# Kernel optimization log

Measured on AMD Instinct MI355X. Metric: run time of the kernel, lower is better.

Reference implementation:

```python
import jax, jax.numpy as jnp
import numpy as np


def setup_inputs() -> dict:
    key = jax.random.key(0)
    x = jax.random.normal(key, (64, 64, 16384), dtype=jnp.float32)
    return {"input_": x, "topk": 128}


def reference(input_, topk):
    # top-k by absolute value along the last axis; zero everything else
    B_shape = input_.shape[:-1]
    L = input_.shape[-1]
    _, idx = jax.lax.top_k(jnp.abs(input_), topk)          # [..., k] indices
    vals = jnp.take_along_axis(input_, idx, axis=-1)        # original signed values
    # flatten leading dims for a single batched scatter
    xf_rows = int(np.prod(B_shape))
    idx2 = idx.reshape(xf_rows, topk)
    vals2 = vals.reshape(xf_rows, topk)
    out = jnp.zeros((xf_rows, L), dtype=input_.dtype)
    rows = jnp.arange(xf_rows)[:, None]
    out = out.at[rows, idx2].set(vals2)
    return out.reshape(*B_shape, L)
```

## Files before the change

kernel.cpp:

```cpp
#include <hip/hip_runtime.h>
#include <stdint.h>

#define ROWLEN 16384
#define NT 512
#define VPT 8

typedef uint32_t uint32x4 __attribute__((ext_vector_type(4)));

#define SYNC_LDS() do { \
    asm volatile("s_waitcnt lgkmcnt(0)" ::: "memory"); \
    __builtin_amdgcn_s_barrier(); \
} while (0)

template <int NB>
__device__ __forceinline__ void select_bin(const uint32_t* __restrict__ hist,
                                           uint32_t* __restrict__ s_part,
                                           uint32_t* s_bin, int* s_kk, int* s_ceq,
                                           int kk, int tid)
{
    constexpr int C = NB / NT;
    uint32_t s = 0;
    #pragma unroll
    for (int j = 0; j < C; ++j) s += hist[tid * C + j];
    s_part[tid] = s;
    SYNC_LDS();
    if (tid < 64) {
        uint32_t g = 0;
        #pragma unroll
        for (int j = 0; j < 8; ++j) g += s_part[tid * 8 + j];
        uint32_t S = g;
        #pragma unroll
        for (int off = 1; off < 64; off <<= 1) {
            uint32_t o = __shfl_down(S, off, 64);
            if (tid + off < 64) S += o;
        }
        unsigned long long m = __ballot(S >= (uint32_t)kk);
        int c = 63 - __builtin_clzll(m);
        uint32_t hv = __shfl(S, (c + 1) & 63, 64);
        uint32_t higher = (c == 63) ? 0u : hv;
        if (tid == 0) {
            uint32_t pp[8];
            #pragma unroll
            for (int j = 0; j < 8; ++j) pp[j] = s_part[c * 8 + j];
            int kk2 = kk - (int)higher;
            int cum = 0, j = 7;
            #pragma unroll
            for (int it = 7; it > 0; --it) {
                int cc = (int)pp[j];
                if (cum + cc >= kk2) break;
                cum += cc; --j;
            }
            int tt = c * 8 + j;
            int kk3 = kk2 - cum;
            uint32_t bb[C];
            #pragma unroll
            for (int jj = 0; jj < C; ++jj) bb[jj] = hist[tt * C + jj];
            int cum2 = 0, b = C - 1;
            #pragma unroll
            for (int it = C - 1; it > 0; --it) {
                int cc = (int)bb[b];
                if (cum2 + cc >= kk3) break;
                cum2 += cc; --b;
            }
            *s_bin = (uint32_t)(tt * C + b);
            *s_kk  = kk3 - cum2;
            *s_ceq = (int)bb[b];
        }
    }
    SYNC_LDS();
}

__global__ __launch_bounds__(NT, 6) void topk_abs_kernel(
    const uint32_t* __restrict__ x, const int* __restrict__ kptr,
    uint32_t* __restrict__ out)
{
    __shared__ uint32_t hist[2048];
    __shared__ uint32_t s_part[NT];
    __shared__ uint32_t s_bin;
    __shared__ int s_kk, s_ceq, s_cnt;

    const int tid = threadIdx.x;
    const uint4* __restrict__ xr  = (const uint4*)(x   + (size_t)blockIdx.x * ROWLEN);
    uint32x4* __restrict__ outr   = (uint32x4*)   (out + (size_t)blockIdx.x * ROWLEN);
    const int k = *kptr;

    uint4 v[VPT];
    #pragma unroll
    for (int i = 0; i < VPT; ++i) v[i] = xr[i * NT + tid];

    hist[tid] = 0; hist[tid + 512] = 0; hist[tid + 1024] = 0; hist[tid + 1536] = 0;
    SYNC_LDS();
    #pragma unroll
    for (int i = 0; i < VPT; ++i) {
        atomicAdd(&hist[(v[i].x & 0x7FFFFFFFu) >> 20], 1u);
        atomicAdd(&hist[(v[i].y & 0x7FFFFFFFu) >> 20], 1u);
        atomicAdd(&hist[(v[i].z & 0x7FFFFFFFu) >> 20], 1u);
        atomicAdd(&hist[(v[i].w & 0x7FFFFFFFu) >> 20], 1u);
    }
    SYNC_LDS();
    select_bin<2048>(hist, s_part, &s_bin, &s_kk, &s_ceq, k, tid);
    const uint32_t b0 = s_bin;
    int kk = s_kk;
    const int ceq0 = s_ceq;

    hist[tid] = 0; hist[tid + 512] = 0;
    if (tid == 0) s_cnt = 0;
    SYNC_LDS();

    uint32_t T; int e, ceqT;
    if (ceq0 <= 1024) {
        uint32_t* cand = hist + 1024;
        #pragma unroll
        for (int i = 0; i < VPT; ++i) {
            uint32_t a;
            a = v[i].x & 0x7FFFFFFFu; if ((a >> 20) == b0) { cand[atomicAdd(&s_cnt, 1)] = a; atomicAdd(&hist[(a >> 10) & 1023u], 1u); }
            a = v[i].y & 0x7FFFFFFFu; if ((a >> 20) == b0) { cand[atomicAdd(&s_cnt, 1)] = a; atomicAdd(&hist[(a >> 10) & 1023u], 1u); }
            a = v[i].z & 0x7FFFFFFFu; if ((a >> 20) == b0) { cand[atomicAdd(&s_cnt, 1)] = a; atomicAdd(&hist[(a >> 10) & 1023u], 1u); }
            a = v[i].w & 0x7FFFFFFFu; if ((a >> 20) == b0) { cand[atomicAdd(&s_cnt, 1)] = a; atomicAdd(&hist[(a >> 10) & 1023u], 1u); }
        }
        SYNC_LDS();
        select_bin<1024>(hist, s_part, &s_bin, &s_kk, &s_ceq, kk, tid);
        const uint32_t b1 = s_bin;
        kk = s_kk;
        hist[tid] = 0; hist[tid + 512] = 0;
        SYNC_LDS();
        for (int t = tid; t < ceq0; t += NT) {
            uint32_t a = cand[t];
            if (((a >> 10) & 1023u) == b1) atomicAdd(&hist[a & 1023u], 1u);
        }
        SYNC_LDS();
        select_bin<1024>(hist, s_part, &s_bin, &s_kk, &s_ceq, kk, tid);
        T = (b0 << 20) | (b1 << 10) | s_bin;
        e = s_kk; ceqT = s_ceq;
    } else {
        #pragma unroll
        for (int i = 0; i < VPT; ++i) {
            uint32_t a;
            a = v[i].x & 0x7FFFFFFFu; if ((a >> 20) == b0) atomicAdd(&hist[(a >> 10) & 1023u], 1u);
            a = v[i].y & 0x7FFFFFFFu; if ((a >> 20) == b0) atomicAdd(&hist[(a >> 10) & 1023u], 1u);
            a = v[i].z & 0x7FFFFFFFu; if ((a >> 20) == b0) atomicAdd(&hist[(a >> 10) & 1023u], 1u);
            a = v[i].w & 0x7FFFFFFFu; if ((a >> 20) == b0) atomicAdd(&hist[(a >> 10) & 1023u], 1u);
        }
        SYNC_LDS();
        select_bin<1024>(hist, s_part, &s_bin, &s_kk, &s_ceq, kk, tid);
        const uint32_t b1 = s_bin;
        kk = s_kk;
        hist[tid] = 0; hist[tid + 512] = 0;
        SYNC_LDS();
        const uint32_t pfx = (b0 << 10) | b1;
        #pragma unroll
        for (int i = 0; i < VPT; ++i) {
            uint32_t a;
            a = v[i].x & 0x7FFFFFFFu; if ((a >> 10) == pfx) atomicAdd(&hist[a & 1023u], 1u);
            a = v[i].y & 0x7FFFFFFFu; if ((a >> 10) == pfx) atomicAdd(&hist[a & 1023u], 1u);
            a = v[i].z & 0x7FFFFFFFu; if ((a >> 10) == pfx) atomicAdd(&hist[a & 1023u], 1u);
            a = v[i].w & 0x7FFFFFFFu; if ((a >> 10) == pfx) atomicAdd(&hist[a & 1023u], 1u);
        }
        SYNC_LDS();
        select_bin<1024>(hist, s_part, &s_bin, &s_kk, &s_ceq, kk, tid);
        T = (b0 << 20) | (b1 << 10) | s_bin;
        e = s_kk; ceqT = s_ceq;
    }

    const bool rare = (ceqT != e);
    int nc = 0;
    if (rare) {
        if (tid == 0) s_cnt = 0;
        SYNC_LDS();
        #pragma unroll
        for (int i = 0; i < VPT; ++i) {
            uint32_t p4 = (uint32_t)(4 * (i * NT + tid));
            if ((v[i].x & 0x7FFFFFFFu) == T) { int q = atomicAdd(&s_cnt, 1); if (q < 1024) hist[q] = p4 + 0u; }
            if ((v[i].y & 0x7FFFFFFFu) == T) { int q = atomicAdd(&s_cnt, 1); if (q < 1024) hist[q] = p4 + 1u; }
            if ((v[i].z & 0x7FFFFFFFu) == T) { int q = atomicAdd(&s_cnt, 1); if (q < 1024) hist[q] = p4 + 2u; }
            if ((v[i].w & 0x7FFFFFFFu) == T) { int q = atomicAdd(&s_cnt, 1); if (q < 1024) hist[q] = p4 + 3u; }
        }
        SYNC_LDS();
        nc = s_cnt; if (nc > 1024) nc = 1024;
        for (int t = tid; t < nc; t += NT) {
            uint32_t my = hist[t];
            int rank = 0;
            for (int j = 0; j < nc; ++j) rank += (hist[j] < my) ? 1 : 0;
            hist[1024 + t] = (rank < e) ? 1u : 0u;
        }
        SYNC_LDS();
    }

    auto filt = [&](uint32_t bits, uint32_t idx) -> uint32_t {
        uint32_t key = bits & 0x7FFFFFFFu;
        if (key > T) return bits;
        if (key < T) return 0u;
        if (!rare) return bits;
        for (int j = 0; j < nc; ++j)
            if (hist[j] == idx) return hist[1024 + j] ? bits : 0u;
        return 0u;
    };
    #pragma unroll
    for (int i = 0; i < VPT; ++i) {
        int p = i * NT + tid;
        uint32_t p4 = (uint32_t)(4 * p);
        uint32x4 o;
        o.x = filt(v[i].x, p4 + 0u);
        o.y = filt(v[i].y, p4 + 1u);
        o.z = filt(v[i].z, p4 + 2u);
        o.w = filt(v[i].w, p4 + 3u);
        __builtin_nontemporal_store(o, &outr[p]);
    }
}

extern "C" void kernel_launch(void* const* d_in, const int* in_sizes, int n_in,
                              void* d_out, int out_size, void* d_ws, size_t ws_size,
                              hipStream_t stream) {
    const uint32_t* x = (const uint32_t*)d_in[0];
    const int* kptr   = (const int*)d_in[1];
    uint32_t* out     = (uint32_t*)d_out;
    const int rows = in_sizes[0] / ROWLEN;
    topk_abs_kernel<<<rows, NT, 0, stream>>>(x, kptr, out);
}
```

Before: 95.62 us.

## Use persistent blocks that prefetch the next row while processing the current

Switches from one block per row to a grid of at most 768 persistent blocks that loop over rows. Each block loads the next row into a second register buffer before running the histogram/select pipeline on the current row, so global load latency overlaps with compute. The cost is doubled register usage for the row data (16 uint4 per thread), which may reduce occupancy or cause spills under the launch bounds, and fewer blocks in flight overall.

```diff
diff --git a/kernel.cpp b/kernel.cpp
--- a/kernel.cpp
+++ b/kernel.cpp
@@ -4,6 +4,7 @@
 #define ROWLEN 16384
 #define NT 512
 #define VPT 8
+#define NBLK 768
 
 typedef uint32_t uint32x4 __attribute__((ext_vector_type(4)));
 
@@ -70,26 +71,22 @@
     SYNC_LDS();
 }
 
-__global__ __launch_bounds__(NT, 6) void topk_abs_kernel(
-    const uint32_t* __restrict__ x, const int* __restrict__ kptr,
-    uint32_t* __restrict__ out)
+struct Shared {
+    uint32_t hist[2048];
+    uint32_t s_part[NT];
+    uint32_t s_bin;
+    int s_kk, s_ceq, s_cnt;
+};
+
+__device__ __forceinline__ void process_row(const uint4 (&v)[VPT], uint32x4* __restrict__ outr,
+                                            int k, int tid, Shared& sh)
 {
-    __shared__ uint32_t hist[2048];
-    __shared__ uint32_t s_part[NT];
-    __shared__ uint32_t s_bin;
-    __shared__ int s_kk, s_ceq, s_cnt;
-
-    const int tid = threadIdx.x;
-    const uint4* __restrict__ xr  = (const uint4*)(x   + (size_t)blockIdx.x * ROWLEN);
-    uint32x4* __restrict__ outr   = (uint32x4*)   (out + (size_t)blockIdx.x * ROWLEN);
-    const int k = *kptr;
-
-    uint4 v[VPT];
-    #pragma unroll
-    for (int i = 0; i < VPT; ++i) v[i] = xr[i * NT + tid];
-
+    uint32_t* hist = sh.hist;
+    SYNC_LDS();
     hist[tid] = 0; hist[tid + 512] = 0; hist[tid + 1024] = 0; hist[tid + 1536] = 0;
-    SYNC_LDS();
+    if (tid == 0) sh.s_cnt = 0;
+    SYNC_LDS();
+
     #pragma unroll
     for (int i = 0; i < VPT; ++i) {
         atomicAdd(&hist[(v[i].x & 0x7FFFFFFFu) >> 20], 1u);
@@ -98,13 +95,12 @@
         atomicAdd(&hist[(v[i].w & 0x7FFFFFFFu) >> 20], 1u);
     }
     SYNC_LDS();
-    select_bin<2048>(hist, s_part, &s_bin, &s_kk, &s_ceq, k, tid);
-    const uint32_t b0 = s_bin;
-    int kk = s_kk;
-    const int ceq0 = s_ceq;
+    select_bin<2048>(hist, sh.s_part, &sh.s_bin, &sh.s_kk, &sh.s_ceq, k, tid);
+    const uint32_t b0 = sh.s_bin;
+    int kk = sh.s_kk;
+    const int ceq0 = sh.s_ceq;
 
     hist[tid] = 0; hist[tid + 512] = 0;
-    if (tid == 0) s_cnt = 0;
     SYNC_LDS();
 
     uint32_t T; int e, ceqT;
@@ -113,15 +109,15 @@
         #pragma unroll
         for (int i = 0; i < VPT; ++i) {
             uint32_t a;
-            a = v[i].x & 0x7FFFFFFFu; if ((a >> 20) == b0) { cand[atomicAdd(&s_cnt, 1)] = a; atomicAdd(&hist[(a >> 10) & 1023u], 1u); }
-            a = v[i].y & 0x7FFFFFFFu; if ((a >> 20) == b0) { cand[atomicAdd(&s_cnt, 1)] = a; atomicAdd(&hist[(a >> 10) & 1023u], 1u); }
-            a = v[i].z & 0x7FFFFFFFu; if ((a >> 20) == b0) { cand[atomicAdd(&s_cnt, 1)] = a; atomicAdd(&hist[(a >> 10) & 1023u], 1u); }
-            a = v[i].w & 0x7FFFFFFFu; if ((a >> 20) == b0) { cand[atomicAdd(&s_cnt, 1)] = a; atomicAdd(&hist[(a >> 10) & 1023u], 1u); }
-        }
-        SYNC_LDS();
-        select_bin<1024>(hist, s_part, &s_bin, &s_kk, &s_ceq, kk, tid);
-        const uint32_t b1 = s_bin;
-        kk = s_kk;
+            a = v[i].x & 0x7FFFFFFFu; if ((a >> 20) == b0) { cand[atomicAdd(&sh.s_cnt, 1)] = a; atomicAdd(&hist[(a >> 10) & 1023u], 1u); }
+            a = v[i].y & 0x7FFFFFFFu; if ((a >> 20) == b0) { cand[atomicAdd(&sh.s_cnt, 1)] = a; atomicAdd(&hist[(a >> 10) & 1023u], 1u); }
+            a = v[i].z & 0x7FFFFFFFu; if ((a >> 20) == b0) { cand[atomicAdd(&sh.s_cnt, 1)] = a; atomicAdd(&hist[(a >> 10) & 1023u], 1u); }
+            a = v[i].w & 0x7FFFFFFFu; if ((a >> 20) == b0) { cand[atomicAdd(&sh.s_cnt, 1)] = a; atomicAdd(&hist[(a >> 10) & 1023u], 1u); }
+        }
+        SYNC_LDS();
+        select_bin<1024>(hist, sh.s_part, &sh.s_bin, &sh.s_kk, &sh.s_ceq, kk, tid);
+        const uint32_t b1 = sh.s_bin;
+        kk = sh.s_kk;
         hist[tid] = 0; hist[tid + 512] = 0;
         SYNC_LDS();
         for (int t = tid; t < ceq0; t += NT) {
@@ -129,9 +125,9 @@
             if (((a >> 10) & 1023u) == b1) atomicAdd(&hist[a & 1023u], 1u);
         }
         SYNC_LDS();
-        select_bin<1024>(hist, s_part, &s_bin, &s_kk, &s_ceq, kk, tid);
-        T = (b0 << 20) | (b1 << 10) | s_bin;
-        e = s_kk; ceqT = s_ceq;
+        select_bin<1024>(hist, sh.s_part, &sh.s_bin, &sh.s_kk, &sh.s_ceq, kk, tid);
+        T = (b0 << 20) | (b1 << 10) | sh.s_bin;
+        e = sh.s_kk; ceqT = sh.s_ceq;
     } else {
         #pragma unroll
         for (int i = 0; i < VPT; ++i) {
@@ -142,9 +138,9 @@
             a = v[i].w & 0x7FFFFFFFu; if ((a >> 20) == b0) atomicAdd(&hist[(a >> 10) & 1023u], 1u);
         }
         SYNC_LDS();
-        select_bin<1024>(hist, s_part, &s_bin, &s_kk, &s_ceq, kk, tid);
-        const uint32_t b1 = s_bin;
-        kk = s_kk;
+        select_bin<1024>(hist, sh.s_part, &sh.s_bin, &sh.s_kk, &sh.s_ceq, kk, tid);
+        const uint32_t b1 = sh.s_bin;
+        kk = sh.s_kk;
         hist[tid] = 0; hist[tid + 512] = 0;
         SYNC_LDS();
         const uint32_t pfx = (b0 << 10) | b1;
@@ -157,26 +153,26 @@
             a = v[i].w & 0x7FFFFFFFu; if ((a >> 10) == pfx) atomicAdd(&hist[a & 1023u], 1u);
         }
         SYNC_LDS();
-        select_bin<1024>(hist, s_part, &s_bin, &s_kk, &s_ceq, kk, tid);
-        T = (b0 << 20) | (b1 << 10) | s_bin;
-        e = s_kk; ceqT = s_ceq;
+        select_bin<1024>(hist, sh.s_part, &sh.s_bin, &sh.s_kk, &sh.s_ceq, kk, tid);
+        T = (b0 << 20) | (b1 << 10) | sh.s_bin;
+        e = sh.s_kk; ceqT = sh.s_ceq;
     }
 
     const bool rare = (ceqT != e);
     int nc = 0;
     if (rare) {
-        if (tid == 0) s_cnt = 0;
+        if (tid == 0) sh.s_cnt = 0;
         SYNC_LDS();
         #pragma unroll
         for (int i = 0; i < VPT; ++i) {
             uint32_t p4 = (uint32_t)(4 * (i * NT + tid));
-            if ((v[i].x & 0x7FFFFFFFu) == T) { int q = atomicAdd(&s_cnt, 1); if (q < 1024) hist[q] = p4 + 0u; }
-            if ((v[i].y & 0x7FFFFFFFu) == T) { int q = atomicAdd(&s_cnt, 1); if (q < 1024) hist[q] = p4 + 1u; }
-            if ((v[i].z & 0x7FFFFFFFu) == T) { int q = atomicAdd(&s_cnt, 1); if (q < 1024) hist[q] = p4 + 2u; }
-            if ((v[i].w & 0x7FFFFFFFu) == T) { int q = atomicAdd(&s_cnt, 1); if (q < 1024) hist[q] = p4 + 3u; }
-        }
-        SYNC_LDS();
-        nc = s_cnt; if (nc > 1024) nc = 1024;
+            if ((v[i].x & 0x7FFFFFFFu) == T) { int q = atomicAdd(&sh.s_cnt, 1); if (q < 1024) hist[q] = p4 + 0u; }
+            if ((v[i].y & 0x7FFFFFFFu) == T) { int q = atomicAdd(&sh.s_cnt, 1); if (q < 1024) hist[q] = p4 + 1u; }
+            if ((v[i].z & 0x7FFFFFFFu) == T) { int q = atomicAdd(&sh.s_cnt, 1); if (q < 1024) hist[q] = p4 + 2u; }
+            if ((v[i].w & 0x7FFFFFFFu) == T) { int q = atomicAdd(&sh.s_cnt, 1); if (q < 1024) hist[q] = p4 + 3u; }
+        }
+        SYNC_LDS();
+        nc = sh.s_cnt; if (nc > 1024) nc = 1024;
         for (int t = tid; t < nc; t += NT) {
             uint32_t my = hist[t];
             int rank = 0;
@@ -208,6 +204,37 @@
     }
 }
 
+__global__ __launch_bounds__(NT, 6) void topk_abs_kernel(
+    const uint32_t* __restrict__ x, const int* __restrict__ kptr,
+    uint32_t* __restrict__ out, int rows, int nblk)
+{
+    __shared__ Shared sh;
+    const int tid = threadIdx.x;
+    const int k = *kptr;
+
+    uint4 va[VPT], vb[VPT];
+    int r = blockIdx.x;
+    if (r >= rows) return;
+
+    const uint4* xr = (const uint4*)(x + (size_t)r * ROWLEN);
+    #pragma unroll
+    for (int i = 0; i < VPT; ++i) va[i] = xr[i * NT + tid];
+
+    for (;;) {
+        int rn = r + nblk;
+        if (rn < rows) {
+            const uint4* xn = (const uint4*)(x + (size_t)rn * ROWLEN);
+            #pragma unroll
+            for (int i = 0; i < VPT; ++i) vb[i] = xn[i * NT + tid];
+        }
+        process_row(va, (uint32x4*)(out + (size_t)r * ROWLEN), k, tid, sh);
+        if (rn >= rows) break;
+        #pragma unroll
+        for (int i = 0; i < VPT; ++i) va[i] = vb[i];
+        r = rn;
+    }
+}
+
 extern "C" void kernel_launch(void* const* d_in, const int* in_sizes, int n_in,
                               void* d_out, int out_size, void* d_ws, size_t ws_size,
                               hipStream_t stream) {
@@ -215,5 +242,6 @@
     const int* kptr   = (const int*)d_in[1];
     uint32_t* out     = (uint32_t*)d_out;
     const int rows = in_sizes[0] / ROWLEN;
-    topk_abs_kernel<<<rows, NT, 0, stream>>>(x, kptr, out);
-}
+    const int nblk = rows < NBLK ? rows : NBLK;
+    topk_abs_kernel<<<nblk, NT, 0, stream>>>(x, kptr, out, rows, nblk);
+}
```

Result: slower. 339.8 us (+255.4%).
